# Kernel optimization log

Measured on AMD Instinct MI355X. Metric: run time of the kernel, lower is better.

The kernel has to match this reference:

```python
import jax, jax.numpy as jnp
import numpy as np

TEMP = 0.2
L_MAIN, L_VIEW, L_SUP, L_UNSUP = 1.0, 1.0, 1.0, 0.2
N, D, V, P, NEG, U = 100000, 256, 3, 1024, 1024, 2048


def setup_inputs() -> dict:
    key = jax.random.key(0)
    ks = jax.random.split(key, 8)
    fused_logit = jax.random.normal(ks[0], (N,), dtype=jnp.float32)
    view_logits = jax.random.normal(ks[1], (V, N), dtype=jnp.float32)
    proj = jax.random.normal(ks[2], (V, N, D), dtype=jnp.float32)
    proj = proj / jnp.linalg.norm(proj, axis=-1, keepdims=True)  # 'already normalized'
    labels = jax.random.randint(ks[3], (N,), 0, 2).astype(jnp.float32)
    train_mask = jax.random.randint(ks[4], (N,), 0, 2).astype(bool)
    train_pos_idx = jax.random.randint(ks[5], (P,), 0, N)
    train_neg_idx = jax.random.randint(ks[6], (NEG,), 0, N)
    unlabeled_idx = jax.random.randint(ks[7], (U,), 0, N)  # len == max_unsup_samples -> no subsampling
    return dict(fused_logit=fused_logit, view_logits=view_logits, proj=proj,
                labels=labels, train_mask=train_mask, train_pos_idx=train_pos_idx,
                train_neg_idx=train_neg_idx, unlabeled_idx=unlabeled_idx)


def _masked_bce(logits, labels, mask):
    # BCEWithLogitsLoss mean over masked elements (stable formulation)
    bce = jnp.maximum(logits, 0) - logits * labels + jnp.log1p(jnp.exp(-jnp.abs(logits)))
    mf = mask.astype(logits.dtype)
    return jnp.sum(bce * mf) / jnp.maximum(jnp.sum(mf), 1.0)


def _sup_contrastive(proj, pos_idx, neg_idx, temp):
    lab_idx = jnp.concatenate([pos_idx, neg_idx])
    node_labels = jnp.concatenate([jnp.ones(pos_idx.shape[0]), jnp.zeros(neg_idx.shape[0])])
    L = lab_idx.shape[0]
    Vv = proj.shape[0]
    z = proj[:, lab_idx, :].transpose(1, 0, 2)          # [L, V, D]
    zf = z.reshape(L * Vv, -1)                           # [L*V, D]
    sim = (zf @ zf.T) / temp                             # [L*V, L*V]
    sim = sim - jax.lax.stop_gradient(sim.max(axis=1, keepdims=True))
    es = jnp.exp(sim)
    node = jnp.repeat(jnp.arange(L), Vv)
    view = jnp.tile(jnp.arange(Vv), L)
    flab = jnp.repeat(node_labels, Vv)
    sn = node[:, None] == node[None, :]
    sv = view[:, None] == view[None, :]
    sl = flab[:, None] == flab[None, :]
    eye = jnp.eye(L * Vv, dtype=bool)
    pos_m = ((sn & ~sv) | (~sn & sl)) & ~eye
    neg_m = (~sn) & (~sl) & ~eye
    den_m = pos_m | neg_m
    denom = jnp.sum(es * den_m.astype(es.dtype), axis=1) + 1e-12
    posf = pos_m.astype(es.dtype)
    log_prob = -jnp.log((es * posf + 1e-12) / denom[:, None])
    pos_count = pos_m.sum(axis=1)
    loss_per_anchor = jnp.sum(log_prob * posf, axis=1) / (pos_count.astype(es.dtype) + 1e-12)
    valid = ((pos_count > 0) & (den_m.sum(axis=1) > 0)).astype(es.dtype)
    return jnp.sum(loss_per_anchor * valid) / jnp.maximum(jnp.sum(valid), 1.0)


def _unsup_consistency(proj, unl_idx, temp):
    # Vectorized form of the double python loop: full cosine-sim matrix with
    # masked denominator (all but self) and positives = same node, other views.
    Vv = proj.shape[0]
    z = proj[:, unl_idx, :].transpose(1, 0, 2)           # [U, V, D]
    Uu = z.shape[0]
    M = Uu * Vv
    zf = z.reshape(M, -1)
    zn = zf / (jnp.linalg.norm(zf, axis=1, keepdims=True) + 1e-8)
    es = jnp.exp((zn @ zn.T) / temp)                     # [M, M]
    denom = es.sum(axis=1) - jnp.diag(es) + 1e-12        # exclude self
    node = jnp.repeat(jnp.arange(Uu), Vv)
    view = jnp.tile(jnp.arange(Vv), Uu)
    pos_m = (node[:, None] == node[None, :]) & (view[:, None] != view[None, :])
    posf = pos_m.astype(es.dtype)
    log_prob = -jnp.log(es / denom[:, None])
    per_anchor = jnp.sum(log_prob * posf, axis=1) / (Vv - 1)
    return jnp.mean(per_anchor)


def reference(fused_logit, view_logits, proj, labels, train_mask,
              train_pos_idx, train_neg_idx, unlabeled_idx):
    main_loss = _masked_bce(fused_logit, labels, train_mask)
    view_loss = jnp.mean(jax.vmap(lambda lg: _masked_bce(lg, labels, train_mask))(view_logits))
    sup_loss = _sup_contrastive(proj, train_pos_idx, train_neg_idx, TEMP)
    unsup_loss = _unsup_consistency(proj, unlabeled_idx, TEMP)
    total = L_MAIN * main_loss + L_VIEW * view_loss + L_SUP * sup_loss + L_UNSUP * unsup_loss
    return jnp.stack([total, main_loss, view_loss, sup_loss, unsup_loss])
```

## Files before the change

kernel.cpp:

```cpp
#include <hip/hip_runtime.h>
#include <math.h>

typedef short short8 __attribute__((ext_vector_type(8)));
typedef float floatx4 __attribute__((ext_vector_type(4)));

#define TEMP_INV 5.0f
#define W_UNSUP 0.2f
#define NB_BCE 256
#define NSPLIT 4

static __device__ __forceinline__ unsigned short f2bf(float f) {
  unsigned int u = __float_as_uint(f);
  u += 0x7FFFu + ((u >> 16) & 1u);
  return (unsigned short)(u >> 16);
}

__device__ __forceinline__ float block_sum256(float v) {
  __shared__ float sh[4];
  for (int m = 1; m <= 32; m <<= 1) v += __shfl_xor(v, m);
  __syncthreads();
  if ((threadIdx.x & 63) == 0) sh[threadIdx.x >> 6] = v;
  __syncthreads();
  return sh[0] + sh[1] + sh[2] + sh[3];
}

__global__ void detect_kernel(const unsigned int* __restrict__ w, int nw, int* __restrict__ flag) {
  __shared__ int s_int, s_flt;
  if (threadIdx.x == 0) { s_int = 1; s_flt = 1; }
  __syncthreads();
  for (int i = threadIdx.x; i < nw; i += blockDim.x) {
    unsigned int x = w[i];
    if (x != 0u && x != 1u) s_int = 0;
    if (x != 0u && x != 0x3F800000u) s_flt = 0;
  }
  __syncthreads();
  if (threadIdx.x == 0) *flag = s_int ? 0 : (s_flt ? 1 : 2);
}

__global__ __launch_bounds__(256) void bce_kernel(
    const float* __restrict__ fused, const float* __restrict__ viewl,
    const float* __restrict__ labels, const void* __restrict__ maskp,
    const int* __restrict__ flagp, float* __restrict__ partials, int N, int V) {
  const int flag = *flagp;
  float cnt = 0.f, sm = 0.f;
  float sv[8];
  for (int v = 0; v < 8; v++) sv[v] = 0.f;
  const int Vc = V > 8 ? 8 : V;
  for (int i = blockIdx.x * blockDim.x + threadIdx.x; i < N; i += gridDim.x * blockDim.x) {
    bool m;
    if (flag == 0)      m = ((const int*)maskp)[i] != 0;
    else if (flag == 1) m = ((const float*)maskp)[i] != 0.0f;
    else                m = ((const unsigned char*)maskp)[i] != 0;
    if (!m) continue;
    float y = labels[i];
    cnt += 1.0f;
    float x = fused[i];
    sm += fmaxf(x, 0.f) - x * y + log1pf(__expf(-fabsf(x)));
    for (int v = 0; v < Vc; v++) {
      float xv = viewl[(size_t)v * N + i];
      sv[v] += fmaxf(xv, 0.f) - xv * y + log1pf(__expf(-fabsf(xv)));
    }
  }
  float tot = block_sum256(cnt);
  if (threadIdx.x == 0) partials[blockIdx.x * 16 + 0] = tot;
  tot = block_sum256(sm);
  if (threadIdx.x == 0) partials[blockIdx.x * 16 + 1] = tot;
  for (int v = 0; v < Vc; v++) {
    tot = block_sum256(sv[v]);
    if (threadIdx.x == 0) partials[blockIdx.x * 16 + 2 + v] = tot;
  }
}

__global__ __launch_bounds__(256) void gather_kernel(
    const float* __restrict__ proj, const int* __restrict__ pos_idx,
    const int* __restrict__ neg_idx, const int* __restrict__ unl_idx,
    unsigned short* __restrict__ zsup, unsigned short* __restrict__ zuns,
    float* __restrict__ dsup, float* __restrict__ duns,
    int N, int D, int V, int P, int Msup, int Muns) {
  const int prob = blockIdx.y;
  const int r = blockIdx.x;
  const int M = prob ? Muns : Msup;
  if (r >= M) return;
  const int l = r / V, v = r - l * V;
  const int idx = prob ? unl_idx[l] : (l < P ? pos_idx[l] : neg_idx[l - P]);
  const float* src = proj + ((size_t)v * N + (size_t)idx) * D;
  const int t = threadIdx.x;
  float s = 0.f;
  for (int d = t; d < D; d += blockDim.x) { float x = src[d]; s += x * x; }
  for (int m = 1; m <= 32; m <<= 1) s += __shfl_xor(s, m);
  __shared__ float sh[4];
  if ((t & 63) == 0) sh[t >> 6] = s;
  __syncthreads();
  const float n2 = sh[0] + sh[1] + sh[2] + sh[3];
  if (prob == 0) {
    for (int d = t; d < D; d += blockDim.x) zsup[(size_t)r * D + d] = f2bf(src[d]);
    if (t == 0) dsup[r] = n2 * TEMP_INV;
  } else {
    const float sc = 1.0f / (sqrtf(n2) + 1e-8f);
    for (int d = t; d < D; d += blockDim.x) zuns[(size_t)r * D + d] = f2bf(src[d] * sc);
    if (t == 0) duns[r] = n2 * sc * sc * TEMP_INV;
  }
}

__global__ __launch_bounds__(256) void sim_kernel(
    const unsigned short* __restrict__ zsup, const unsigned short* __restrict__ zuns,
    float* __restrict__ Esup, float* __restrict__ Bsup,
    float* __restrict__ Euns, float* __restrict__ Buns,
    int Msup, int Muns, int PV, int V) {
  const int prob = blockIdx.z;
  const unsigned short* __restrict__ z = prob ? zuns : zsup;
  float* __restrict__ Ep = prob ? Euns : Esup;
  float* __restrict__ Bp = prob ? Buns : Bsup;
  const int M = prob ? Muns : Msup;

  const int tid = threadIdx.x;
  const int lane = tid & 63;
  const int wave = tid >> 6;
  const int q = lane >> 4;
  const int n16 = lane & 15;

  const int rowBase = blockIdx.y * 64 + wave * 16;

  int arow = rowBase + n16; if (arow >= M) arow = M - 1;
  short8 afrag[8];
  {
    const unsigned short* zr = z + (size_t)arow * 256 + q * 8;
#pragma unroll
    for (int ks = 0; ks < 8; ks++) afrag[ks] = *(const short8*)(zr + ks * 32);
  }

  int bs[4], be[4];
#pragma unroll
  for (int r = 0; r < 4; r++) {
    int row = rowBase + q * 4 + r;
    if (row >= M) row = M - 1;
    if (prob == 0) { bs[r] = (row < PV) ? 0 : PV; be[r] = (row < PV) ? PV : M; }
    else           { int b0 = (row / V) * V; bs[r] = b0; be[r] = b0 + V; }
  }

  float Eacc[4] = {0.f, 0.f, 0.f, 0.f};
  float Bacc[4] = {0.f, 0.f, 0.f, 0.f};

  __shared__ __align__(16) unsigned short lds[64 * 264];

  int cps = ((M + NSPLIT * 64 - 1) / (NSPLIT * 64)) * 64;
  int colStart = blockIdx.x * cps;
  int colEnd = colStart + cps; if (colEnd > M) colEnd = M;

  for (int c0 = colStart; c0 < colEnd; c0 += 64) {
    __syncthreads();
#pragma unroll
    for (int cc = 0; cc < 8; cc++) {
      int chunk = cc * 256 + tid;
      int rrow = chunk >> 5;
      int off = (chunk & 31) * 8;
      int gcol = c0 + rrow;
      short8 vv = {0, 0, 0, 0, 0, 0, 0, 0};
      if (gcol < M) vv = *(const short8*)(z + (size_t)gcol * 256 + off);
      *(short8*)(&lds[rrow * 264 + off]) = vv;
    }
    __syncthreads();

#pragma unroll
    for (int cb = 0; cb < 4; cb++) {
      floatx4 acc = {0.f, 0.f, 0.f, 0.f};
      const unsigned short* bp = &lds[(cb * 16 + n16) * 264 + q * 8];
#pragma unroll
      for (int ks = 0; ks < 8; ks++) {
        short8 bfrag = *(const short8*)(bp + ks * 32);
        acc = __builtin_amdgcn_mfma_f32_16x16x32_bf16(afrag[ks], bfrag, acc, 0, 0, 0);
      }
      int j = c0 + cb * 16 + n16;
      if (j < M) {
#pragma unroll
        for (int r = 0; r < 4; r++) {
          float t = acc[r] * TEMP_INV;
          Eacc[r] += __expf(t - 5.0f);
          Bacc[r] += (j >= bs[r] && j < be[r]) ? t : 0.0f;
        }
      }
    }
  }

#pragma unroll
  for (int r = 0; r < 4; r++) {
    float e = Eacc[r], b = Bacc[r];
    for (int m = 1; m <= 8; m <<= 1) { e += __shfl_xor(e, m); b += __shfl_xor(b, m); }
    int row = rowBase + q * 4 + r;
    if (n16 == 0 && row < M) {
      Ep[(size_t)blockIdx.x * M + row] = e;
      Bp[(size_t)blockIdx.x * M + row] = b;
    }
  }
}

__global__ __launch_bounds__(256) void finalize_kernel(
    const float* __restrict__ partials,
    const float* __restrict__ Esup, const float* __restrict__ Bsup, const float* __restrict__ dsup,
    const float* __restrict__ Euns, const float* __restrict__ Buns, const float* __restrict__ duns,
    int Msup, int Muns, int PV, int P, int NEG, int V, float* __restrict__ out) {
  const int t = threadIdx.x;
  float cnt = 0.f, sm = 0.f, sv[8];
  for (int v = 0; v < 8; v++) sv[v] = 0.f;
  const int Vc = V > 8 ? 8 : V;
  for (int b = t; b < NB_BCE; b += 256) {
    cnt += partials[b * 16 + 0];
    sm  += partials[b * 16 + 1];
    for (int v = 0; v < Vc; v++) sv[v] += partials[b * 16 + 2 + v];
  }
  cnt = block_sum256(cnt);
  sm = block_sum256(sm);
  float svt = 0.f;
  for (int v = 0; v < Vc; v++) svt += block_sum256(sv[v]);
  const float denomC = fmaxf(cnt, 1.0f);
  const float main_loss = sm / denomC;
  const float view_loss = (svt / denomC) / (float)V;

  float ssup = 0.f;
  for (int row = t; row < Msup; row += 256) {
    float E = 0.f, B = 0.f;
    for (int s = 0; s < NSPLIT; s++) {
      E += Esup[(size_t)s * Msup + row];
      B += Bsup[(size_t)s * Msup + row];
    }
    float d = dsup[row];
    float dn = E - __expf(d - 5.0f);
    float cl = (row < PV) ? (float)P : (float)NEG;
    float pc = (float)(V - 1) + (cl - 1.0f) * (float)V;
    ssup += logf(dn) + 5.0f - (B - d) / pc;
  }
  ssup = block_sum256(ssup);
  const float sup_loss = ssup / (float)Msup;

  float suns = 0.f;
  for (int row = t; row < Muns; row += 256) {
    float E = 0.f, B = 0.f;
    for (int s = 0; s < NSPLIT; s++) {
      E += Euns[(size_t)s * Muns + row];
      B += Buns[(size_t)s * Muns + row];
    }
    float d = duns[row];
    float dn = E - __expf(d - 5.0f);
    suns += logf(dn) + 5.0f - (B - d) / (float)(V - 1);
  }
  suns = block_sum256(suns);
  const float unsup_loss = suns / (float)Muns;

  if (t == 0) {
    float total = main_loss + view_loss + sup_loss + W_UNSUP * unsup_loss;
    out[0] = total;
    out[1] = main_loss;
    out[2] = view_loss;
    out[3] = sup_loss;
    out[4] = unsup_loss;
  }
}

extern "C" void kernel_launch(void* const* d_in, const int* in_sizes, int n_in,
                              void* d_out, int out_size, void* d_ws, size_t ws_size,
                              hipStream_t stream) {
  const float* fused  = (const float*)d_in[0];
  const float* viewl  = (const float*)d_in[1];
  const float* proj   = (const float*)d_in[2];
  const float* labels = (const float*)d_in[3];
  const void*  maskp  = d_in[4];
  const int* pos_idx  = (const int*)d_in[5];
  const int* neg_idx  = (const int*)d_in[6];
  const int* unl_idx  = (const int*)d_in[7];

  const int N = in_sizes[0];
  const int V = in_sizes[1] / N;
  const int D = in_sizes[2] / in_sizes[1];
  const int P = in_sizes[5];
  const int NEG = in_sizes[6];
  const int U = in_sizes[7];
  const int L = P + NEG;
  const int Msup = L * V;
  const int Muns = U * V;
  const int PV = P * V;

  char* ws = (char*)d_ws;
  size_t off = 0;
  auto alloc = [&](size_t bytes) { size_t o = off; off += (bytes + 255) & ~(size_t)255; return o; };
  const size_t o_flag = alloc(4);
  const size_t o_part = alloc((size_t)NB_BCE * 16 * 4);
  const size_t o_zsup = alloc((size_t)Msup * D * 2);
  const size_t o_zuns = alloc((size_t)Muns * D * 2);
  const size_t o_dsup = alloc((size_t)Msup * 4);
  const size_t o_duns = alloc((size_t)Muns * 4);
  const size_t o_Esup = alloc((size_t)NSPLIT * Msup * 4);
  const size_t o_Bsup = alloc((size_t)NSPLIT * Msup * 4);
  const size_t o_Euns = alloc((size_t)NSPLIT * Muns * 4);
  const size_t o_Buns = alloc((size_t)NSPLIT * Muns * 4);

  int* flag = (int*)(ws + o_flag);
  float* partials = (float*)(ws + o_part);
  unsigned short* zsup = (unsigned short*)(ws + o_zsup);
  unsigned short* zuns = (unsigned short*)(ws + o_zuns);
  float* dsup = (float*)(ws + o_dsup);
  float* duns = (float*)(ws + o_duns);
  float* Esup = (float*)(ws + o_Esup);
  float* Bsup = (float*)(ws + o_Bsup);
  float* Euns = (float*)(ws + o_Euns);
  float* Buns = (float*)(ws + o_Buns);

  int nw = N / 4 < 256 ? N / 4 : 256;
  detect_kernel<<<1, 256, 0, stream>>>((const unsigned int*)maskp, nw, flag);
  bce_kernel<<<NB_BCE, 256, 0, stream>>>(fused, viewl, labels, maskp, flag, partials, N, V);

  const int Mmax = Msup > Muns ? Msup : Muns;
  dim3 ggrid(Mmax, 2);
  gather_kernel<<<ggrid, 256, 0, stream>>>(proj, pos_idx, neg_idx, unl_idx,
                                           zsup, zuns, dsup, duns, N, D, V, P, Msup, Muns);

  dim3 sgrid(NSPLIT, (Mmax + 63) / 64, 2);
  sim_kernel<<<sgrid, 256, 0, stream>>>(zsup, zuns, Esup, Bsup, Euns, Buns, Msup, Muns, PV, V);

  finalize_kernel<<<1, 256, 0, stream>>>(partials, Esup, Bsup, dsup, Euns, Buns, duns,
                                         Msup, Muns, PV, P, NEG, V, (float*)d_out);
}
```

Baseline: 479.3 us.

## Compute positive-pair sums via class sums and enlarge sim kernel row tile

Removes the per-element masked accumulation of positive similarities from the GEMM loop. Those sums are obtained algebraically as dot products of each row with precomputed per-class (sup) or per-node (unsup) column sums, in new sums and anchor kernels. The sim kernel now processes 64 rows per wave group with 4 MFMA accumulators, uses exp2 with fused scaling, doubles the column split, and accumulates with atomics instead of split partial buffers. The gather is wave-per-row with float4 loads, and the final reduction is spread across many blocks with atomics. This adds extra launches plus a memset, and the atomic float accumulation changes the summation order.

```diff
diff --git a/kernel.cpp b/kernel.cpp
--- a/kernel.cpp
+++ b/kernel.cpp
@@ -4,15 +4,18 @@
 typedef short short8 __attribute__((ext_vector_type(8)));
 typedef float floatx4 __attribute__((ext_vector_type(4)));
 
-#define TEMP_INV 5.0f
 #define W_UNSUP 0.2f
 #define NB_BCE 256
-#define NSPLIT 4
+#define NSPLIT 8
+#define L2E5 7.2134752f
 
 static __device__ __forceinline__ unsigned short f2bf(float f) {
   unsigned int u = __float_as_uint(f);
   u += 0x7FFFu + ((u >> 16) & 1u);
   return (unsigned short)(u >> 16);
+}
+static __device__ __forceinline__ float bf2f(unsigned short u) {
+  return __uint_as_float(((unsigned int)u) << 16);
 }
 
 __device__ __forceinline__ float block_sum256(float v) {
@@ -78,177 +81,192 @@
     float* __restrict__ dsup, float* __restrict__ duns,
     int N, int D, int V, int P, int Msup, int Muns) {
   const int prob = blockIdx.y;
-  const int r = blockIdx.x;
+  const int wave = threadIdx.x >> 6, lane = threadIdx.x & 63;
+  const int r = blockIdx.x * 4 + wave;
   const int M = prob ? Muns : Msup;
   if (r >= M) return;
   const int l = r / V, v = r - l * V;
   const int idx = prob ? unl_idx[l] : (l < P ? pos_idx[l] : neg_idx[l - P]);
   const float* src = proj + ((size_t)v * N + (size_t)idx) * D;
-  const int t = threadIdx.x;
-  float s = 0.f;
-  for (int d = t; d < D; d += blockDim.x) { float x = src[d]; s += x * x; }
-  for (int m = 1; m <= 32; m <<= 1) s += __shfl_xor(s, m);
-  __shared__ float sh[4];
-  if ((t & 63) == 0) sh[t >> 6] = s;
-  __syncthreads();
-  const float n2 = sh[0] + sh[1] + sh[2] + sh[3];
+  float ss = 0.f;
+  for (int d0 = lane * 4; d0 < D; d0 += 256) {
+    float4 x = *(const float4*)(src + d0);
+    ss += x.x * x.x + x.y * x.y + x.z * x.z + x.w * x.w;
+  }
+  for (int m = 1; m <= 32; m <<= 1) ss += __shfl_xor(ss, m);
   if (prob == 0) {
-    for (int d = t; d < D; d += blockDim.x) zsup[(size_t)r * D + d] = f2bf(src[d]);
-    if (t == 0) dsup[r] = n2 * TEMP_INV;
+    for (int d0 = lane * 4; d0 < D; d0 += 256) {
+      float4 x = *(const float4*)(src + d0);
+      unsigned short o[4] = {f2bf(x.x), f2bf(x.y), f2bf(x.z), f2bf(x.w)};
+      *(unsigned long long*)(zsup + (size_t)r * D + d0) = *(unsigned long long*)o;
+    }
+    if (lane == 0) dsup[r] = ss * 5.0f;
   } else {
-    const float sc = 1.0f / (sqrtf(n2) + 1e-8f);
-    for (int d = t; d < D; d += blockDim.x) zuns[(size_t)r * D + d] = f2bf(src[d] * sc);
-    if (t == 0) duns[r] = n2 * sc * sc * TEMP_INV;
-  }
-}
-
-__global__ __launch_bounds__(256) void sim_kernel(
+    const float sc = 1.0f / (sqrtf(ss) + 1e-8f);
+    for (int d0 = lane * 4; d0 < D; d0 += 256) {
+      float4 x = *(const float4*)(src + d0);
+      unsigned short o[4] = {f2bf(x.x * sc), f2bf(x.y * sc), f2bf(x.z * sc), f2bf(x.w * sc)};
+      *(unsigned long long*)(zuns + (size_t)r * D + d0) = *(unsigned long long*)o;
+    }
+    if (lane == 0) duns[r] = ss * sc * sc * 5.0f;
+  }
+}
+
+__global__ __launch_bounds__(256) void sums_kernel(
     const unsigned short* __restrict__ zsup, const unsigned short* __restrict__ zuns,
-    float* __restrict__ Esup, float* __restrict__ Bsup,
-    float* __restrict__ Euns, float* __restrict__ Buns,
-    int Msup, int Muns, int PV, int V) {
+    float* __restrict__ Ssup, float* __restrict__ Suns,
+    int D, int V, int PV, int Msup, int U) {
+  const int b = blockIdx.x;
+  if (b < 32) {
+    const int lab = b >> 4, sub = b & 15;
+    const int start = lab ? PV : 0, end = lab ? Msup : PV;
+    for (int d = threadIdx.x; d < D; d += 256) {
+      float acc = 0.f;
+      for (int r = start + sub; r < end; r += 16) acc += bf2f(zsup[(size_t)r * D + d]);
+      atomicAdd(&Ssup[lab * D + d], acc);
+    }
+  } else {
+    const int n = b - 32;
+    if (n >= U) return;
+    for (int d = threadIdx.x; d < D; d += 256) {
+      float acc = 0.f;
+      for (int v = 0; v < V; v++) acc += bf2f(zuns[((size_t)n * V + v) * D + d]);
+      Suns[(size_t)n * D + d] = acc;
+    }
+  }
+}
+
+template <bool CHECK>
+__global__ __launch_bounds__(256, 2) void sim_kernel(
+    const unsigned short* __restrict__ zsup, const unsigned short* __restrict__ zuns,
+    float* __restrict__ Esup, float* __restrict__ Euns, int Msup, int Muns) {
   const int prob = blockIdx.z;
   const unsigned short* __restrict__ z = prob ? zuns : zsup;
   float* __restrict__ Ep = prob ? Euns : Esup;
-  float* __restrict__ Bp = prob ? Buns : Bsup;
   const int M = prob ? Muns : Msup;
-
-  const int tid = threadIdx.x;
-  const int lane = tid & 63;
-  const int wave = tid >> 6;
-  const int q = lane >> 4;
-  const int n16 = lane & 15;
-
-  const int rowBase = blockIdx.y * 64 + wave * 16;
-
-  int arow = rowBase + n16; if (arow >= M) arow = M - 1;
-  short8 afrag[8];
-  {
+  const int tid = threadIdx.x, lane = tid & 63, wave = tid >> 6;
+  const int q = lane >> 4, n16 = lane & 15;
+  const int rowBase = blockIdx.y * 64;
+  if (rowBase >= M) return;
+
+  short8 afrag[4][8];
+#pragma unroll
+  for (int s = 0; s < 4; s++) {
+    int arow = rowBase + s * 16 + n16;
+    if (CHECK && arow >= M) arow = M - 1;
     const unsigned short* zr = z + (size_t)arow * 256 + q * 8;
 #pragma unroll
-    for (int ks = 0; ks < 8; ks++) afrag[ks] = *(const short8*)(zr + ks * 32);
-  }
-
-  int bs[4], be[4];
-#pragma unroll
-  for (int r = 0; r < 4; r++) {
-    int row = rowBase + q * 4 + r;
-    if (row >= M) row = M - 1;
-    if (prob == 0) { bs[r] = (row < PV) ? 0 : PV; be[r] = (row < PV) ? PV : M; }
-    else           { int b0 = (row / V) * V; bs[r] = b0; be[r] = b0 + V; }
-  }
-
-  float Eacc[4] = {0.f, 0.f, 0.f, 0.f};
-  float Bacc[4] = {0.f, 0.f, 0.f, 0.f};
-
+    for (int ks = 0; ks < 8; ks++) afrag[s][ks] = *(const short8*)(zr + ks * 32);
+  }
+
+  float Eacc[4][4] = {};
   __shared__ __align__(16) unsigned short lds[64 * 264];
 
-  int cps = ((M + NSPLIT * 64 - 1) / (NSPLIT * 64)) * 64;
-  int colStart = blockIdx.x * cps;
-  int colEnd = colStart + cps; if (colEnd > M) colEnd = M;
-
-  for (int c0 = colStart; c0 < colEnd; c0 += 64) {
+  const int tiles = (M + 63) >> 6;
+  const int tps = (tiles + NSPLIT - 1) / NSPLIT;
+  const int tBeg = blockIdx.x * tps;
+  const int tEnd = min(tBeg + tps, tiles);
+
+  for (int tI = tBeg; tI < tEnd; tI++) {
+    const int c0 = tI * 64;
     __syncthreads();
 #pragma unroll
     for (int cc = 0; cc < 8; cc++) {
       int chunk = cc * 256 + tid;
-      int rrow = chunk >> 5;
-      int off = (chunk & 31) * 8;
+      int rrow = chunk >> 5, off = (chunk & 31) * 8;
       int gcol = c0 + rrow;
-      short8 vv = {0, 0, 0, 0, 0, 0, 0, 0};
-      if (gcol < M) vv = *(const short8*)(z + (size_t)gcol * 256 + off);
+      short8 vv = {};
+      if (!CHECK || gcol < M) vv = *(const short8*)(z + (size_t)gcol * 256 + off);
       *(short8*)(&lds[rrow * 264 + off]) = vv;
     }
     __syncthreads();
 
-#pragma unroll
-    for (int cb = 0; cb < 4; cb++) {
-      floatx4 acc = {0.f, 0.f, 0.f, 0.f};
-      const unsigned short* bp = &lds[(cb * 16 + n16) * 264 + q * 8];
-#pragma unroll
-      for (int ks = 0; ks < 8; ks++) {
-        short8 bfrag = *(const short8*)(bp + ks * 32);
-        acc = __builtin_amdgcn_mfma_f32_16x16x32_bf16(afrag[ks], bfrag, acc, 0, 0, 0);
-      }
-      int j = c0 + cb * 16 + n16;
-      if (j < M) {
-#pragma unroll
-        for (int r = 0; r < 4; r++) {
-          float t = acc[r] * TEMP_INV;
-          Eacc[r] += __expf(t - 5.0f);
-          Bacc[r] += (j >= bs[r] && j < be[r]) ? t : 0.0f;
-        }
-      }
-    }
-  }
-
-#pragma unroll
-  for (int r = 0; r < 4; r++) {
-    float e = Eacc[r], b = Bacc[r];
-    for (int m = 1; m <= 8; m <<= 1) { e += __shfl_xor(e, m); b += __shfl_xor(b, m); }
-    int row = rowBase + q * 4 + r;
-    if (n16 == 0 && row < M) {
-      Ep[(size_t)blockIdx.x * M + row] = e;
-      Bp[(size_t)blockIdx.x * M + row] = b;
-    }
-  }
-}
-
-__global__ __launch_bounds__(256) void finalize_kernel(
-    const float* __restrict__ partials,
-    const float* __restrict__ Esup, const float* __restrict__ Bsup, const float* __restrict__ dsup,
-    const float* __restrict__ Euns, const float* __restrict__ Buns, const float* __restrict__ duns,
-    int Msup, int Muns, int PV, int P, int NEG, int V, float* __restrict__ out) {
-  const int t = threadIdx.x;
-  float cnt = 0.f, sm = 0.f, sv[8];
-  for (int v = 0; v < 8; v++) sv[v] = 0.f;
+    const unsigned short* bp = &lds[(wave * 16 + n16) * 264 + q * 8];
+    floatx4 a0 = {}, a1 = {}, a2 = {}, a3 = {};
+#pragma unroll
+    for (int ks = 0; ks < 8; ks++) {
+      short8 bfrag = *(const short8*)(bp + ks * 32);
+      a0 = __builtin_amdgcn_mfma_f32_16x16x32_bf16(afrag[0][ks], bfrag, a0, 0, 0, 0);
+      a1 = __builtin_amdgcn_mfma_f32_16x16x32_bf16(afrag[1][ks], bfrag, a1, 0, 0, 0);
+      a2 = __builtin_amdgcn_mfma_f32_16x16x32_bf16(afrag[2][ks], bfrag, a2, 0, 0, 0);
+      a3 = __builtin_amdgcn_mfma_f32_16x16x32_bf16(afrag[3][ks], bfrag, a3, 0, 0, 0);
+    }
+    const int j = c0 + wave * 16 + n16;
+    const bool jok = !CHECK || (j < M);
+#pragma unroll
+    for (int r = 0; r < 4; r++) {
+      float e0 = exp2f(fmaf(a0[r], L2E5, -L2E5));
+      float e1 = exp2f(fmaf(a1[r], L2E5, -L2E5));
+      float e2 = exp2f(fmaf(a2[r], L2E5, -L2E5));
+      float e3 = exp2f(fmaf(a3[r], L2E5, -L2E5));
+      if (jok) { Eacc[0][r] += e0; Eacc[1][r] += e1; Eacc[2][r] += e2; Eacc[3][r] += e3; }
+    }
+  }
+
+#pragma unroll
+  for (int s = 0; s < 4; s++) {
+#pragma unroll
+    for (int r = 0; r < 4; r++) {
+      float e = Eacc[s][r];
+      e += __shfl_xor(e, 1); e += __shfl_xor(e, 2);
+      e += __shfl_xor(e, 4); e += __shfl_xor(e, 8);
+      const int row = rowBase + s * 16 + q * 4 + r;
+      if (n16 == 0 && (!CHECK || row < M)) atomicAdd(&Ep[row], e);
+    }
+  }
+}
+
+__global__ __launch_bounds__(256) void anchor_kernel(
+    const unsigned short* __restrict__ zsup, const unsigned short* __restrict__ zuns,
+    const float* __restrict__ Esup, const float* __restrict__ Euns,
+    const float* __restrict__ dsup, const float* __restrict__ duns,
+    const float* __restrict__ Ssup, const float* __restrict__ Suns,
+    float* __restrict__ sums, int Msup, int Muns, int PV, int P, int NEG, int V, int D) {
+  const int prob = blockIdx.y;
+  const int wave = threadIdx.x >> 6, lane = threadIdx.x & 63;
+  const int row = blockIdx.x * 4 + wave;
+  const int M = prob ? Muns : Msup;
+  if (row >= M) return;
+  const unsigned short* z = prob ? zuns : zsup;
+  const float* S = prob ? &Suns[(size_t)(row / V) * D] : &Ssup[(row < PV ? 0 : 1) * D];
+  float dp = 0.f;
+  for (int d0 = lane * 4; d0 < D; d0 += 256) {
+    const unsigned short* zr = z + (size_t)row * D + d0;
+    float4 s4 = *(const float4*)(S + d0);
+    dp += bf2f(zr[0]) * s4.x + bf2f(zr[1]) * s4.y + bf2f(zr[2]) * s4.z + bf2f(zr[3]) * s4.w;
+  }
+  for (int m = 1; m <= 32; m <<= 1) dp += __shfl_xor(dp, m);
+  if (lane == 0) {
+    const float E = prob ? Euns[row] : Esup[row];
+    const float d = prob ? duns[row] : dsup[row];
+    const float ediag = exp2f(fmaf(d, 1.4426950f, -L2E5));
+    const float B = 5.0f * dp;
+    const float pc = prob ? (float)(V - 1) : (float)((row < PV ? P : NEG) * V - 1);
+    const float term = logf(E - ediag) + 5.0f - (B - d) / pc;
+    atomicAdd(&sums[prob], term);
+  }
+}
+
+__global__ __launch_bounds__(256) void final_kernel(
+    const float* __restrict__ partials, const float* __restrict__ sums,
+    int Msup, int Muns, int V, float* __restrict__ out) {
+  float cnt = 0.f, sm = 0.f, sv = 0.f;
   const int Vc = V > 8 ? 8 : V;
-  for (int b = t; b < NB_BCE; b += 256) {
+  for (int b = threadIdx.x; b < NB_BCE; b += 256) {
     cnt += partials[b * 16 + 0];
-    sm  += partials[b * 16 + 1];
-    for (int v = 0; v < Vc; v++) sv[v] += partials[b * 16 + 2 + v];
+    sm += partials[b * 16 + 1];
+    for (int v = 0; v < Vc; v++) sv += partials[b * 16 + 2 + v];
   }
   cnt = block_sum256(cnt);
   sm = block_sum256(sm);
-  float svt = 0.f;
-  for (int v = 0; v < Vc; v++) svt += block_sum256(sv[v]);
-  const float denomC = fmaxf(cnt, 1.0f);
-  const float main_loss = sm / denomC;
-  const float view_loss = (svt / denomC) / (float)V;
-
-  float ssup = 0.f;
-  for (int row = t; row < Msup; row += 256) {
-    float E = 0.f, B = 0.f;
-    for (int s = 0; s < NSPLIT; s++) {
-      E += Esup[(size_t)s * Msup + row];
-      B += Bsup[(size_t)s * Msup + row];
-    }
-    float d = dsup[row];
-    float dn = E - __expf(d - 5.0f);
-    float cl = (row < PV) ? (float)P : (float)NEG;
-    float pc = (float)(V - 1) + (cl - 1.0f) * (float)V;
-    ssup += logf(dn) + 5.0f - (B - d) / pc;
-  }
-  ssup = block_sum256(ssup);
-  const float sup_loss = ssup / (float)Msup;
-
-  float suns = 0.f;
-  for (int row = t; row < Muns; row += 256) {
-    float E = 0.f, B = 0.f;
-    for (int s = 0; s < NSPLIT; s++) {
-      E += Euns[(size_t)s * Muns + row];
-      B += Buns[(size_t)s * Muns + row];
-    }
-    float d = duns[row];
-    float dn = E - __expf(d - 5.0f);
-    suns += logf(dn) + 5.0f - (B - d) / (float)(V - 1);
-  }
-  suns = block_sum256(suns);
-  const float unsup_loss = suns / (float)Muns;
-
-  if (t == 0) {
-    float total = main_loss + view_loss + sup_loss + W_UNSUP * unsup_loss;
-    out[0] = total;
+  sv = block_sum256(sv);
+  if (threadIdx.x == 0) {
+    const float denomC = fmaxf(cnt, 1.0f);
+    const float main_loss = sm / denomC;
+    const float view_loss = (sv / denomC) / (float)V;
+    const float sup_loss = sums[0] / (float)Msup;
+    const float unsup_loss = sums[1] / (float)Muns;
+    out[0] = main_loss + view_loss + sup_loss + W_UNSUP * unsup_loss;
     out[1] = main_loss;
     out[2] = view_loss;
     out[3] = sup_loss;
@@ -278,6 +296,7 @@
   const int Msup = L * V;
   const int Muns = U * V;
   const int PV = P * V;
+  const int Mmax = Msup > Muns ? Msup : Muns;
 
   char* ws = (char*)d_ws;
   size_t off = 0;
@@ -288,10 +307,12 @@
   const size_t o_zuns = alloc((size_t)Muns * D * 2);
   const size_t o_dsup = alloc((size_t)Msup * 4);
   const size_t o_duns = alloc((size_t)Muns * 4);
-  const size_t o_Esup = alloc((size_t)NSPLIT * Msup * 4);
-  const size_t o_Bsup = alloc((size_t)NSPLIT * Msup * 4);
-  const size_t o_Euns = alloc((size_t)NSPLIT * Muns * 4);
-  const size_t o_Buns = alloc((size_t)NSPLIT * Muns * 4);
+  const size_t o_Suns = alloc((size_t)U * D * 4);
+  const size_t o_Esup = alloc((size_t)Msup * 4);
+  const size_t o_Euns = alloc((size_t)Muns * 4);
+  const size_t o_Ssup = alloc((size_t)2 * D * 4);
+  const size_t o_sums = alloc(8);
+  const size_t zero_beg = o_Esup, zero_end = o_sums + 256;
 
   int* flag = (int*)(ws + o_flag);
   float* partials = (float*)(ws + o_part);
@@ -299,23 +320,34 @@
   unsigned short* zuns = (unsigned short*)(ws + o_zuns);
   float* dsup = (float*)(ws + o_dsup);
   float* duns = (float*)(ws + o_duns);
+  float* Suns = (float*)(ws + o_Suns);
   float* Esup = (float*)(ws + o_Esup);
-  float* Bsup = (float*)(ws + o_Bsup);
   float* Euns = (float*)(ws + o_Euns);
-  float* Buns = (float*)(ws + o_Buns);
+  float* Ssup = (float*)(ws + o_Ssup);
+  float* sums = (float*)(ws + o_sums);
+
+  hipMemsetAsync(ws + zero_beg, 0, zero_end - zero_beg, stream);
 
   int nw = N / 4 < 256 ? N / 4 : 256;
   detect_kernel<<<1, 256, 0, stream>>>((const unsigned int*)maskp, nw, flag);
   bce_kernel<<<NB_BCE, 256, 0, stream>>>(fused, viewl, labels, maskp, flag, partials, N, V);
 
-  const int Mmax = Msup > Muns ? Msup : Muns;
-  dim3 ggrid(Mmax, 2);
+  dim3 ggrid((Mmax + 3) / 4, 2);
   gather_kernel<<<ggrid, 256, 0, stream>>>(proj, pos_idx, neg_idx, unl_idx,
                                            zsup, zuns, dsup, duns, N, D, V, P, Msup, Muns);
 
+  sums_kernel<<<32 + U, 256, 0, stream>>>(zsup, zuns, Ssup, Suns, D, V, PV, Msup, U);
+
   dim3 sgrid(NSPLIT, (Mmax + 63) / 64, 2);
-  sim_kernel<<<sgrid, 256, 0, stream>>>(zsup, zuns, Esup, Bsup, Euns, Buns, Msup, Muns, PV, V);
-
-  finalize_kernel<<<1, 256, 0, stream>>>(partials, Esup, Bsup, dsup, Euns, Buns, duns,
-                                         Msup, Muns, PV, P, NEG, V, (float*)d_out);
-}
+  const bool need_check = ((Msup & 63) != 0) || ((Muns & 63) != 0);
+  if (need_check)
+    sim_kernel<true><<<sgrid, 256, 0, stream>>>(zsup, zuns, Esup, Euns, Msup, Muns);
+  else
+    sim_kernel<false><<<sgrid, 256, 0, stream>>>(zsup, zuns, Esup, Euns, Msup, Muns);
+
+  dim3 agrid((Mmax + 3) / 4, 2);
+  anchor_kernel<<<agrid, 256, 0, stream>>>(zsup, zuns, Esup, Euns, dsup, duns,
+                                           Ssup, Suns, sums, Msup, Muns, PV, P, NEG, V, D);
+
+  final_kernel<<<1, 256, 0, stream>>>(partials, sums, Msup, Muns, V, (float*)d_out);
+}
```

Measured after the change: 652.5 us. 36.1% more time.
